# Performance work log

Hardware: AMD Instinct MI355X
Metric: run time of the kernel (lower is better)

## Reference

```python
import jax, jax.numpy as jnp
import numpy as np

B, T, DKQ, DV, EKQ, EV, H, OUT = 8, 2048, 64, 64, 128, 128, 4, 32
FF = 4 * EV
NEG = -1e30  # additive mask value (safe stand-in for -inf)


def _ln(x, g, b, eps=1e-5):
    m = x.mean(-1, keepdims=True)
    var = ((x - m) ** 2).mean(-1, keepdims=True)
    return (x - m) * jax.lax.rsqrt(var + eps) * g + b


def _attn(q, k, v, mask):
    # q,k,v: [n, T, E] -> heads [n, H, T, dh]; NOTE: no 1/sqrt(d) scaling (faithful to source)
    n, t, _ = q.shape
    q = q.reshape(n, t, H, -1).transpose(0, 2, 1, 3)
    k = k.reshape(n, t, H, -1).transpose(0, 2, 1, 3)
    v = v.reshape(n, t, H, -1).transpose(0, 2, 1, 3)
    w = jnp.einsum('bhqd,bhkd->bhqk', q, k) + mask  # [n,H,T,T]
    a = jax.nn.softmax(w, axis=-1)
    o = jnp.einsum('bhqk,bhkd->bhqd', a, v)
    return o.transpose(0, 2, 1, 3).reshape(n, t, -1)


def setup_inputs() -> dict:
    key = jax.random.key(0)
    ks = jax.random.split(key, 32)
    w = lambda k, s: jax.random.normal(k, s, jnp.float32) * 0.02
    DIN_A = DKQ + DV
    return {
        'kq': jax.random.normal(ks[0], (B, T, DKQ), jnp.float32),
        'v': jax.random.normal(ks[1], (B, T, DV), jnp.float32),
        # Layer A (input_dim = DKQ+DV, embed = EV)
        'A_Wk': w(ks[2], (DIN_A, EV)), 'A_bk': jnp.zeros((EV,), jnp.float32),
        'A_Wq': w(ks[3], (DIN_A, EV)), 'A_bq': jnp.zeros((EV,), jnp.float32),
        'A_Wv': w(ks[4], (DIN_A, EV)), 'A_bv': jnp.zeros((EV,), jnp.float32),
        'A_f1W': w(ks[5], (EV, FF)), 'A_f1b': jnp.zeros((FF,), jnp.float32),
        'A_f2W': w(ks[6], (FF, EV)), 'A_f2b': jnp.zeros((EV,), jnp.float32),
        'A_n1g': jnp.ones((EV,), jnp.float32), 'A_n1b': jnp.zeros((EV,), jnp.float32),
        'A_n2g': jnp.ones((EV,), jnp.float32), 'A_n2b': jnp.zeros((EV,), jnp.float32),
        # Layer B (kq -> EKQ, vA -> EV)
        'B_Wk': w(ks[7], (DKQ, EKQ)), 'B_bk': jnp.zeros((EKQ,), jnp.float32),
        'B_Wq': w(ks[8], (DKQ, EKQ)), 'B_bq': jnp.zeros((EKQ,), jnp.float32),
        'B_Wv': w(ks[9], (EV, EV)), 'B_bv': jnp.zeros((EV,), jnp.float32),
        'B_f1W': w(ks[10], (EV, FF)), 'B_f1b': jnp.zeros((FF,), jnp.float32),
        'B_f2W': w(ks[11], (FF, EV)), 'B_f2b': jnp.zeros((EV,), jnp.float32),
        # Output head
        'out_W': w(ks[12], (EV, OUT)), 'out_b': jnp.zeros((OUT,), jnp.float32),
    }


def reference(kq, v, A_Wk, A_bk, A_Wq, A_bq, A_Wv, A_bv, A_f1W, A_f1b, A_f2W, A_f2b,
              A_n1g, A_n1b, A_n2g, A_n2b, B_Wk, B_bk, B_Wq, B_bq, B_Wv, B_bv,
              B_f1W, B_f1b, B_f2W, B_f2b, out_W, out_b):
    n, t, _ = kq.shape
    i = jnp.arange(t)[:, None]
    j = jnp.arange(t)[None, :]
    mask_a = jnp.where(j <= i, 0.0, NEG).astype(jnp.float32)               # causal (diag=1)
    mask_b = jnp.where((j < i) | ((i == 0) & (j == 0)), 0.0, NEG).astype(jnp.float32)  # strict causal + (0,0) exception

    # ---- Layer A ----
    X = jnp.concatenate([kq, v], axis=-1)
    K = X @ A_Wk + A_bk
    Q = X @ A_Wq + A_bq
    V = X @ A_Wv + A_bv
    attn_out = _attn(Q, K, V, mask_a)
    h1 = _ln(V + attn_out, A_n1g, A_n1b)
    ff = jax.nn.gelu(h1 @ A_f1W + A_f1b, approximate=False) @ A_f2W + A_f2b
    vA = _ln(h1 + ff, A_n2g, A_n2b)

    # ---- Layer B (no residuals / norms: values is overwritten in source) ----
    K2 = kq @ B_Wk + B_bk
    Q2 = kq @ B_Wq + B_bq
    V2 = vA @ B_Wv + B_bv
    attn_out2 = _attn(Q2, K2, V2, mask_b)
    ff2 = jax.nn.gelu(attn_out2 @ B_f1W + B_f1b, approximate=False) @ B_f2W + B_f2b

    return ff2 @ out_W + out_b
```

## Files before the change

kernel.cpp:

```cpp
#include <hip/hip_runtime.h>
#include <hip/hip_bf16.h>

#define TSEQ 2048
#define NBATCH 8
#define NROWS (NBATCH*TSEQ)
#define EMB 128
#define NH 4
#define DH 32
#define OUTD 32
#define APLANE (NROWS*EMB)
#define LOG2E 1.4426950408889634f

typedef short s8v __attribute__((ext_vector_type(8)));
typedef short s4v __attribute__((ext_vector_type(4)));
typedef float f4v __attribute__((ext_vector_type(4)));

__device__ __forceinline__ unsigned short f2bf(float f){
  unsigned int u = __float_as_uint(f);
  unsigned int r = u + 0x7fffu + ((u >> 16) & 1u);
  return (unsigned short)(r >> 16);
}
__device__ __forceinline__ float bf2f(unsigned short u){
  return __uint_as_float(((unsigned int)u) << 16);
}

struct WPack {
  const float* src[10];
  int off[10];
  int ntk[10];
  int rowoff[10];
  int nsh[10];
  int kn[10];
};
__global__ __launch_bounds__(256) void prep_w(WPack p, short* __restrict__ warena){
  int blk = blockIdx.x, m = 0;
  #pragma unroll
  for (int i=0;i<10;i++){
    int nb = p.kn[i] >> 8;
    if (blk < nb){ m = i; break; }
    blk -= nb;
  }
  int idx = blk*256 + threadIdx.x;
  float x = p.src[m][idx];
  int nsh = p.nsh[m];
  int n = idx & ((1<<nsh)-1);
  int k = idx >> nsh;
  int K = p.kn[m] >> nsh;
  unsigned short hi = f2bf(x);
  unsigned short lo = f2bf(x - bf2f(hi));
  short* dh = warena + p.off[m] + (size_t)(p.rowoff[m] + n)*K + k;
  dh[0]        = (short)hi;
  dh[p.ntk[m]] = (short)lo;
}

__global__ __launch_bounds__(256) void prep_wc(const float* __restrict__ f2W, const float* __restrict__ f2b,
                                               const float* __restrict__ oW, const float* __restrict__ ob,
                                               float* __restrict__ Wc, float* __restrict__ bc){
  int idx = blockIdx.x*256 + threadIdx.x;
  if (idx < 512*32){
    int k = idx >> 5, n = idx & 31;
    float s = 0.f;
    #pragma unroll 4
    for (int j=0;j<128;j++) s = fmaf(f2W[k*128+j], oW[j*32+n], s);
    Wc[idx] = s;
  } else if (idx < 512*32 + 32){
    int n = idx - 512*32;
    float s = ob[n];
    for (int j=0;j<128;j++) s = fmaf(f2b[j], oW[j*32+n], s);
    bc[n] = s;
  }
}

__global__ __launch_bounds__(256) void xsplit(const float* __restrict__ kq, const float* __restrict__ v,
                                              unsigned short* __restrict__ X){
  int idx = blockIdx.x*256 + threadIdx.x;
  int row = idx >> 7, c = idx & 127;
  float val = (c < 64) ? kq[row*64 + c] : v[row*64 + (c-64)];
  unsigned short hi = f2bf(val);
  X[idx]          = hi;
  X[idx + APLANE] = f2bf(val - bf2f(hi));
}

struct GOuts {
  const float* bias[3];
  float* of[3];
  unsigned short* ob[3];
  unsigned short* vt[3];
  float scale[3];
};
__global__ __launch_bounds__(256) void gemm2(
    const unsigned short* __restrict__ A, int aplane, int lda, int K, int niter,
    const short* __restrict__ wt, int NTK,
    GOuts og, int NT, int nseg, int act){
  __shared__ short As[2][2][64*40];
  const int tid  = threadIdx.x;
  const int w    = tid >> 6;
  const int lane = tid & 63;
  const int col  = lane & 15;
  const int quad = lane >> 4;
  const int row0 = blockIdx.x * 64;
  const int colg = blockIdx.y*64 + w*16 + col;
  const bool two = (aplane != 0);

  f4v acc[4];
  #pragma unroll
  for (int i=0;i<4;i++) acc[i] = (f4v){0.f,0.f,0.f,0.f};

  const int ar = tid >> 2, ac = (tid & 3)*8;
  const unsigned short* abase = A + (size_t)(row0 + ar)*lda;
  const short* wbase = wt + (size_t)colg*K + quad*8;

  s8v pah, pal, pbh, pbl;
  pah = *(const s8v*)(abase + ac);
  if (two) pal = *(const s8v*)(abase + aplane + ac);
  pbh = *(const s8v*)(wbase);
  pbl = *(const s8v*)(wbase + NTK);

  for (int i=0;i<niter;i++){
    const int buf = i & 1;
    *(s8v*)&As[buf][0][ar*40 + ac] = pah;
    if (two) *(s8v*)&As[buf][1][ar*40 + ac] = pal;
    __syncthreads();
    s8v bh = pbh, bl = pbl;
    if (i+1 < niter){
      const int kcol = (i+1)*32;
      pah = *(const s8v*)(abase + kcol + ac);
      if (two) pal = *(const s8v*)(abase + aplane + kcol + ac);
      pbh = *(const s8v*)(wbase + kcol);
      pbl = *(const s8v*)(wbase + NTK + kcol);
    }
    #pragma unroll
    for (int rt=0;rt<4;rt++){
      s8v ah = *(const s8v*)&As[buf][0][(rt*16 + col)*40 + quad*8];
      acc[rt] = __builtin_amdgcn_mfma_f32_16x16x32_bf16(ah, bh, acc[rt], 0, 0, 0);
      if (two){
        s8v al = *(const s8v*)&As[buf][1][(rt*16 + col)*40 + quad*8];
        acc[rt] = __builtin_amdgcn_mfma_f32_16x16x32_bf16(al, bh, acc[rt], 0, 0, 0);
      }
      acc[rt] = __builtin_amdgcn_mfma_f32_16x16x32_bf16(ah, bl, acc[rt], 0, 0, 0);
    }
  }

  int seg, lcol, ldc;
  if (nseg > 1){ seg = colg >> 7; lcol = colg & 127; ldc = 128; }
  else         { seg = 0; lcol = colg; ldc = NT; }
  const float bv = og.bias[seg][lcol];
  const float sc = og.scale[seg];
  float* of = og.of[seg];
  unsigned short* ob = og.ob[seg];
  unsigned short* vtp = og.vt[seg];
  float vals[4][4];
  #pragma unroll
  for (int rt=0;rt<4;rt++){
    #pragma unroll
    for (int r=0;r<4;r++){
      float val = acc[rt][r] + bv;
      if (act == 1) val = 0.5f*val*(1.f + erff(val*0.70710678118654752440f));
      vals[rt][r] = val * sc;
    }
  }
  #pragma unroll
  for (int rt=0;rt<4;rt++){
    const int row = row0 + rt*16 + quad*4;
    #pragma unroll
    for (int r=0;r<4;r++){
      if (ob)      ob[(size_t)(row+r)*ldc + lcol] = f2bf(vals[rt][r]);
      else if (of) of[(size_t)(row+r)*ldc + lcol] = vals[rt][r];
    }
  }
  if (vtp){
    const int hh = lcol >> 5, dd = lcol & 31;
    const int bb = row0 >> 11;
    unsigned short* vbase = vtp + ((size_t)(bb*NH + hh)*32 + dd)*TSEQ + (row0 & (TSEQ-1)) + quad*4;
    #pragma unroll
    for (int rt=0;rt<4;rt++){
      s4v pk;
      #pragma unroll
      for (int r=0;r<4;r++) pk[r] = (short)f2bf(vals[rt][r]);
      *(s4v*)(vbase + rt*16) = pk;
    }
  }
}

#define KT_STRIDE 40
#define VT_STRIDE 72
#define PW_STRIDE 72
__global__ __launch_bounds__(128) void flash3(const unsigned short* __restrict__ Qb,
                                              const unsigned short* __restrict__ Kb,
                                              const unsigned short* __restrict__ Vtb,
                                              float* __restrict__ O0, float* __restrict__ O1,
                                              float* __restrict__ L0, float* __restrict__ L1,
                                              int mode){
  __shared__ short Kt[64*KT_STRIDE];
  __shared__ short Vt[32*VT_STRIDE];
  __shared__ short Pw[2][16*PW_STRIDE];
  const int tid  = threadIdx.x;
  const int w    = tid >> 6;
  const int lane = tid & 63;
  const int col  = lane & 15;
  const int quad = lane >> 4;
  const int bh = blockIdx.y;
  const int b = bh >> 2, h = bh & 3;
  const int par = blockIdx.z;
  float* Op = par ? O1 : O0;
  float* Lp = par ? L1 : L0;
  const int kr = tid >> 1, kc16 = (tid & 1)*16;
  const int vd = tid >> 2, vk16 = (tid & 3)*16;

  for (int pass = 0; pass < 2; pass++){
    const int t = pass ? blockIdx.x : (63 - blockIdx.x);
    const int qbase = t*32 + w*16;
    const int jtmax = t >> 1;
    const int qg = qbase + col;

    s8v qf = *(const s8v*)(Qb + (size_t)(b*TSEQ + qg)*EMB + h*DH + quad*8);
    f4v o0 = {0.f,0.f,0.f,0.f}, o1 = {0.f,0.f,0.f,0.f};
    float lsum = 0.f;

    if (par <= jtmax){
      s8v ka, kb2, va, vb;
      {
        const unsigned short* kp = Kb + (size_t)(b*TSEQ + par*64 + kr)*EMB + h*DH + kc16;
        ka = *(const s8v*)kp; kb2 = *(const s8v*)(kp + 8);
        const unsigned short* vp = Vtb + ((size_t)bh*32 + vd)*TSEQ + par*64 + vk16;
        va = *(const s8v*)vp; vb = *(const s8v*)(vp + 8);
      }
      for (int jt = par; jt <= jtmax; jt += 2){
        __syncthreads();
        *(s8v*)&Kt[kr*KT_STRIDE + kc16]     = ka;
        *(s8v*)&Kt[kr*KT_STRIDE + kc16 + 8] = kb2;
        *(s8v*)&Vt[vd*VT_STRIDE + vk16]     = va;
        *(s8v*)&Vt[vd*VT_STRIDE + vk16 + 8] = vb;
        __syncthreads();
        if (jt + 2 <= jtmax){
          const unsigned short* kp = Kb + (size_t)(b*TSEQ + (jt+2)*64 + kr)*EMB + h*DH + kc16;
          ka = *(const s8v*)kp; kb2 = *(const s8v*)(kp + 8);
          const unsigned short* vp = Vtb + ((size_t)bh*32 + vd)*TSEQ + (jt+2)*64 + vk16;
          va = *(const s8v*)vp; vb = *(const s8v*)(vp + 8);
        }
        f4v s[4];
        #pragma unroll
        for (int t4=0;t4<4;t4++){
          s8v kf = *(const s8v*)&Kt[(t4*16 + col)*KT_STRIDE + quad*8];
          f4v z = {0.f,0.f,0.f,0.f};
          s[t4] = __builtin_amdgcn_mfma_f32_16x16x32_bf16(kf, qf, z, 0, 0, 0);
        }
        if (jt == jtmax){
          const int j0 = jt*64;
          #pragma unroll
          for (int t4=0;t4<4;t4++){
            #pragma unroll
            for (int r=0;r<4;r++){
              const int jg = j0 + t4*16 + quad*4 + r;
              const bool ok = (mode==0) ? (jg <= qg) : ((jg < qg) || (qg==0 && jg==0));
              s[t4][r] = ok ? s[t4][r] : -1e30f;
            }
          }
        }
        #pragma unroll
        for (int t4=0;t4<4;t4++){
          s4v pk;
          #pragma unroll
          for (int r=0;r<4;r++){
            float pv = exp2f(s[t4][r]);
            lsum += pv;
            pk[r] = (short)f2bf(pv);
          }
          *(s4v*)&Pw[w][col*PW_STRIDE + t4*16 + quad*4] = pk;
        }
        #pragma unroll
        for (int kk=0;kk<2;kk++){
          s8v pf  = *(const s8v*)&Pw[w][col*PW_STRIDE + kk*32 + quad*8];
          s8v vf0 = *(const s8v*)&Vt[(col)*VT_STRIDE    + kk*32 + quad*8];
          s8v vf1 = *(const s8v*)&Vt[(16+col)*VT_STRIDE + kk*32 + quad*8];
          o0 = __builtin_amdgcn_mfma_f32_16x16x32_bf16(vf0, pf, o0, 0, 0, 0);
          o1 = __builtin_amdgcn_mfma_f32_16x16x32_bf16(vf1, pf, o1, 0, 0, 0);
        }
      }
    }
    lsum += __shfl_xor(lsum, 16);
    lsum += __shfl_xor(lsum, 32);
    float* obase = Op + (size_t)(b*TSEQ + qg)*EMB + h*DH + quad*4;
    *(float4*)(obase)      = make_float4(o0[0],o0[1],o0[2],o0[3]);
    *(float4*)(obase + 16) = make_float4(o1[0],o1[1],o1[2],o1[3]);
    if (quad == 0) Lp[(size_t)(b*TSEQ + qg)*NH + h] = lsum;
  }
}

__global__ __launch_bounds__(64) void combine_ln(const float* __restrict__ O0, const float* __restrict__ O1,
                                                 const float* __restrict__ L0, const float* __restrict__ L1,
                                                 const float* __restrict__ Vf,
                                                 const float* __restrict__ g, const float* __restrict__ bt,
                                                 unsigned short* __restrict__ outp){
  const int row = blockIdx.x;
  const int tid = threadIdx.x;
  const size_t base = (size_t)row*EMB;
  const int h0 = tid >> 5, h1i = 2 + (tid >> 5);
  const float la = L0[(size_t)row*NH + h0] + L1[(size_t)row*NH + h0];
  const float lb = L0[(size_t)row*NH + h1i] + L1[(size_t)row*NH + h1i];
  float x0 = Vf[base+tid]    + (O0[base+tid]    + O1[base+tid])    / la;
  float x1 = Vf[base+tid+64] + (O0[base+tid+64] + O1[base+tid+64]) / lb;
  float s  = x0 + x1;
  float s2 = x0*x0 + x1*x1;
  #pragma unroll
  for (int off=1; off<64; off<<=1){
    s  += __shfl_xor(s,  off);
    s2 += __shfl_xor(s2, off);
  }
  float mean = s * (1.f/128.f);
  float var  = s2 * (1.f/128.f) - mean*mean;
  float rstd = rsqrtf(var + 1e-5f);
  float y0 = (x0-mean)*rstd*g[tid]    + bt[tid];
  float y1 = (x1-mean)*rstd*g[tid+64] + bt[tid+64];
  unsigned short h0b = f2bf(y0), h1b = f2bf(y1);
  outp[base+tid]             = h0b;
  outp[base+tid+64]          = h1b;
  outp[base+tid+APLANE]      = f2bf(y0 - bf2f(h0b));
  outp[base+tid+64+APLANE]   = f2bf(y1 - bf2f(h1b));
}

__global__ __launch_bounds__(64) void ln2(const unsigned short* __restrict__ Xp, const float* __restrict__ R,
                                          const float* __restrict__ g, const float* __restrict__ bt,
                                          unsigned short* __restrict__ outp){
  const int row = blockIdx.x;
  const int tid = threadIdx.x;
  const size_t base = (size_t)row*EMB;
  float x0 = bf2f(Xp[base+tid])    + bf2f(Xp[base+tid+APLANE])    + R[base+tid];
  float x1 = bf2f(Xp[base+tid+64]) + bf2f(Xp[base+tid+64+APLANE]) + R[base+tid+64];
  float s  = x0 + x1;
  float s2 = x0*x0 + x1*x1;
  #pragma unroll
  for (int off=1; off<64; off<<=1){
    s  += __shfl_xor(s,  off);
    s2 += __shfl_xor(s2, off);
  }
  float mean = s * (1.f/128.f);
  float var  = s2 * (1.f/128.f) - mean*mean;
  float rstd = rsqrtf(var + 1e-5f);
  float y0 = (x0-mean)*rstd*g[tid]    + bt[tid];
  float y1 = (x1-mean)*rstd*g[tid+64] + bt[tid+64];
  unsigned short h0b = f2bf(y0), h1b = f2bf(y1);
  outp[base+tid]             = h0b;
  outp[base+tid+64]          = h1b;
  outp[base+tid+APLANE]      = f2bf(y0 - bf2f(h0b));
  outp[base+tid+64+APLANE]   = f2bf(y1 - bf2f(h1b));
}

__global__ __launch_bounds__(256) void combine_b(const float* __restrict__ O0, const float* __restrict__ O1,
                                                 const float* __restrict__ L0, const float* __restrict__ L1,
                                                 unsigned short* __restrict__ outp){
  const int idx = blockIdx.x*256 + threadIdx.x;
  const int row = idx >> 7, c = idx & 127, h = c >> 5;
  const float l = L0[(size_t)row*NH + h] + L1[(size_t)row*NH + h];
  const float v = (O0[idx] + O1[idx]) / l;
  unsigned short hb = f2bf(v);
  outp[idx]          = hb;
  outp[idx + APLANE] = f2bf(v - bf2f(hb));
}

__global__ __launch_bounds__(256) void out2(const unsigned short* __restrict__ mid,
                                            const float* __restrict__ Wc, const float* __restrict__ bc,
                                            float* __restrict__ out){
  __shared__ float As[8*512];
  const int tid = threadIdx.x;
  const int row0 = blockIdx.x*8;
  for (int idx = tid; idx < 8*512; idx += 256)
    As[idx] = bf2f(mid[(size_t)row0*512 + idx]);
  __syncthreads();
  const int r = tid >> 5, c = tid & 31;
  float acc = bc[c];
  const float* as = &As[r*512];
  #pragma unroll 8
  for (int k=0;k<512;k++) acc = fmaf(as[k], Wc[k*32+c], acc);
  out[(size_t)(row0+r)*OUTD + c] = acc;
}

extern "C" void kernel_launch(void* const* d_in, const int* in_sizes, int n_in,
                              void* d_out, int out_size, void* d_ws, size_t ws_size,
                              hipStream_t stream) {
  const float* kq    = (const float*)d_in[0];
  const float* v     = (const float*)d_in[1];
  const float* A_Wk  = (const float*)d_in[2];  const float* A_bk  = (const float*)d_in[3];
  const float* A_Wq  = (const float*)d_in[4];  const float* A_bq  = (const float*)d_in[5];
  const float* A_Wv  = (const float*)d_in[6];  const float* A_bv  = (const float*)d_in[7];
  const float* A_f1W = (const float*)d_in[8];  const float* A_f1b = (const float*)d_in[9];
  const float* A_f2W = (const float*)d_in[10]; const float* A_f2b = (const float*)d_in[11];
  const float* A_n1g = (const float*)d_in[12]; const float* A_n1b = (const float*)d_in[13];
  const float* A_n2g = (const float*)d_in[14]; const float* A_n2b = (const float*)d_in[15];
  const float* B_Wk  = (const float*)d_in[16]; const float* B_bk  = (const float*)d_in[17];
  const float* B_Wq  = (const float*)d_in[18]; const float* B_bq  = (const float*)d_in[19];
  const float* B_Wv  = (const float*)d_in[20]; const float* B_bv  = (const float*)d_in[21];
  const float* B_f1W = (const float*)d_in[22]; const float* B_f1b = (const float*)d_in[23];
  const float* B_f2W = (const float*)d_in[24]; const float* B_f2b = (const float*)d_in[25];
  const float* out_W = (const float*)d_in[26]; const float* out_b = (const float*)d_in[27];
  float* out = (float*)d_out;
  (void)in_sizes; (void)n_in; (void)out_size; (void)ws_size;

  char* ws = (char*)d_ws;
  const size_t MB = 1024*1024;
  short* warena = (short*)ws;
  float* Wc  = (float*)(ws + 1536*1024);
  float* bc  = (float*)(ws + 1536*1024 + 65536);
  unsigned short* Xs  = (unsigned short*)(ws + 2*MB);
  unsigned short* Qbf = (unsigned short*)(ws + 10*MB);
  unsigned short* Kbf = (unsigned short*)(ws + 14*MB);
  unsigned short* Vtb = (unsigned short*)(ws + 18*MB);
  float* Vf  = (float*)(ws + 22*MB);
  float* O0  = (float*)(ws + 30*MB);
  float* O1  = (float*)(ws + 38*MB);
  float* L0  = (float*)(ws + 46*MB);
  float* L1  = (float*)(ws + 47*MB);
  unsigned short* h1p = (unsigned short*)(ws + 48*MB);
  unsigned short* mid = (unsigned short*)(ws + 56*MB);
  float* ffo = (float*)(ws + 72*MB);
  unsigned short* vAp = (unsigned short*)(ws + 80*MB);

  WPack p;
  const float* srcs[10] = {A_Wq,A_Wk,A_Wv,A_f1W,A_f2W,B_Wq,B_Wk,B_Wv,B_f1W,B_f2W};
  int kn[10]     = {16384,16384,16384,65536,65536,8192,8192,16384,65536,65536};
  int nsh[10]    = {7,7,7,9,7,7,7,7,9,7};
  int off[10]    = {0,0,0,98304,229376,360448,360448,393216,425984,557056};
  int ntk[10]    = {49152,49152,49152,65536,65536,16384,16384,16384,65536,65536};
  int rowoff[10] = {0,128,256,0,0,0,128,0,0,0};
  int nblk = 0;
  for (int i=0;i<10;i++){
    p.src[i]=srcs[i]; p.kn[i]=kn[i]; p.nsh[i]=nsh[i];
    p.off[i]=off[i]; p.ntk[i]=ntk[i]; p.rowoff[i]=rowoff[i];
    nblk += kn[i] >> 8;
  }
  prep_w<<<nblk, 256, 0, stream>>>(p, warena);
  prep_wc<<<65, 256, 0, stream>>>(B_f2W, B_f2b, out_W, out_b, Wc, bc);
  xsplit<<<NROWS*128/256, 256, 0, stream>>>(kq, v, Xs);

  GOuts oQKVA = {{A_bq,A_bk,A_bv},{nullptr,nullptr,Vf},{Qbf,Kbf,nullptr},{nullptr,nullptr,Vtb},{LOG2E,1.f,1.f}};
  GOuts oF1A  = {{A_f1b,nullptr,nullptr},{nullptr,nullptr,nullptr},{mid,nullptr,nullptr},{nullptr,nullptr,nullptr},{1.f,1.f,1.f}};
  GOuts oF2A  = {{A_f2b,nullptr,nullptr},{ffo,nullptr,nullptr},{nullptr,nullptr,nullptr},{nullptr,nullptr,nullptr},{1.f,1.f,1.f}};
  GOuts oQKB  = {{B_bq,B_bk,nullptr},{nullptr,nullptr,nullptr},{Qbf,Kbf,nullptr},{nullptr,nullptr,nullptr},{LOG2E,1.f,1.f}};
  GOuts oVB   = {{B_bv,nullptr,nullptr},{nullptr,nullptr,nullptr},{nullptr,nullptr,nullptr},{Vtb,nullptr,nullptr},{1.f,1.f,1.f}};
  GOuts oF1B  = {{B_f1b,nullptr,nullptr},{nullptr,nullptr,nullptr},{mid,nullptr,nullptr},{nullptr,nullptr,nullptr},{1.f,1.f,1.f}};

  gemm2<<<dim3(256,6), 256, 0, stream>>>(Xs, APLANE, 128, 128, 4, warena + 0,      49152, oQKVA, 384, 3, 0);
  flash3<<<dim3(32,32,2), 128, 0, stream>>>(Qbf, Kbf, Vtb, O0, O1, L0, L1, 0);
  combine_ln<<<NROWS, 64, 0, stream>>>(O0, O1, L0, L1, Vf, A_n1g, A_n1b, h1p);
  gemm2<<<dim3(256,8), 256, 0, stream>>>(h1p, APLANE, 128, 128, 4, warena + 98304, 65536, oF1A, 512, 1, 1);
  gemm2<<<dim3(256,2), 256, 0, stream>>>(mid, 0,      512, 512, 16, warena + 229376, 65536, oF2A, 128, 1, 0);
  ln2<<<NROWS, 64, 0, stream>>>(h1p, ffo, A_n2g, A_n2b, vAp);

  gemm2<<<dim3(256,4), 256, 0, stream>>>(Xs, APLANE, 128, 64, 2,  warena + 360448, 16384, oQKB, 256, 2, 0);
  gemm2<<<dim3(256,2), 256, 0, stream>>>(vAp, APLANE, 128, 128, 4, warena + 393216, 16384, oVB, 128, 1, 0);
  flash3<<<dim3(32,32,2), 128, 0, stream>>>(Qbf, Kbf, Vtb, O0, O1, L0, L1, 1);
  combine_b<<<NROWS*128/256, 256, 0, stream>>>(O0, O1, L0, L1, h1p);
  gemm2<<<dim3(256,8), 256, 0, stream>>>(h1p, APLANE, 128, 128, 4, warena + 425984, 65536, oF1B, 512, 1, 1);
  out2<<<NROWS/8, 256, 0, stream>>>(mid, Wc, bc, out);
}
```

Measured before the change: 333.1 us.

## Merge prep kernels, move V transpose to separate kernel, compute row sums via MFMA

The three setup kernels (weight split, combined output weights, input split) are merged into one launch to cut launch overhead. The GEMM epilogue no longer writes the transposed V with scattered stores; it writes row-major bf16 V, and a new LDS-based transpose kernel produces the transposed layout. In the flash kernel the softmax row sums are computed with an extra MFMA against a ones vector instead of scalar adds and shuffles, and packing uses paired bf16 conversion. Workspace buffers are also remapped to reuse regions. This adds two small kernel launches and one extra MFMA per tile.

```diff
diff --git a/kernel.cpp b/kernel.cpp
--- a/kernel.cpp
+++ b/kernel.cpp
@@ -12,7 +12,6 @@
 #define LOG2E 1.4426950408889634f
 
 typedef short s8v __attribute__((ext_vector_type(8)));
-typedef short s4v __attribute__((ext_vector_type(4)));
 typedef float f4v __attribute__((ext_vector_type(4)));
 
 __device__ __forceinline__ unsigned short f2bf(float f){
@@ -32,60 +31,62 @@
   int nsh[10];
   int kn[10];
 };
-__global__ __launch_bounds__(256) void prep_w(WPack p, short* __restrict__ warena){
-  int blk = blockIdx.x, m = 0;
-  #pragma unroll
-  for (int i=0;i<10;i++){
-    int nb = p.kn[i] >> 8;
-    if (blk < nb){ m = i; break; }
-    blk -= nb;
-  }
-  int idx = blk*256 + threadIdx.x;
-  float x = p.src[m][idx];
-  int nsh = p.nsh[m];
-  int n = idx & ((1<<nsh)-1);
-  int k = idx >> nsh;
-  int K = p.kn[m] >> nsh;
-  unsigned short hi = f2bf(x);
-  unsigned short lo = f2bf(x - bf2f(hi));
-  short* dh = warena + p.off[m] + (size_t)(p.rowoff[m] + n)*K + k;
-  dh[0]        = (short)hi;
-  dh[p.ntk[m]] = (short)lo;
-}
-
-__global__ __launch_bounds__(256) void prep_wc(const float* __restrict__ f2W, const float* __restrict__ f2b,
-                                               const float* __restrict__ oW, const float* __restrict__ ob,
-                                               float* __restrict__ Wc, float* __restrict__ bc){
-  int idx = blockIdx.x*256 + threadIdx.x;
-  if (idx < 512*32){
-    int k = idx >> 5, n = idx & 31;
-    float s = 0.f;
-    #pragma unroll 4
-    for (int j=0;j<128;j++) s = fmaf(f2W[k*128+j], oW[j*32+n], s);
-    Wc[idx] = s;
-  } else if (idx < 512*32 + 32){
-    int n = idx - 512*32;
-    float s = ob[n];
-    for (int j=0;j<128;j++) s = fmaf(f2b[j], oW[j*32+n], s);
-    bc[n] = s;
-  }
-}
-
-__global__ __launch_bounds__(256) void xsplit(const float* __restrict__ kq, const float* __restrict__ v,
-                                              unsigned short* __restrict__ X){
-  int idx = blockIdx.x*256 + threadIdx.x;
-  int row = idx >> 7, c = idx & 127;
-  float val = (c < 64) ? kq[row*64 + c] : v[row*64 + (c-64)];
-  unsigned short hi = f2bf(val);
-  X[idx]          = hi;
-  X[idx + APLANE] = f2bf(val - bf2f(hi));
+struct PrepArgs {
+  const float* f2W; const float* f2b; const float* oW; const float* ob;
+  float* Wc; float* bc;
+  const float* kq; const float* v;
+  unsigned short* X;
+  int nblk_w;
+};
+__global__ __launch_bounds__(256) void prep_all(WPack p, PrepArgs a, short* __restrict__ warena){
+  int bid = blockIdx.x;
+  if (bid < a.nblk_w){
+    int blk = bid, m = 0;
+    #pragma unroll
+    for (int i=0;i<10;i++){
+      int nb = p.kn[i] >> 8;
+      if (blk < nb){ m = i; break; }
+      blk -= nb;
+    }
+    int idx = blk*256 + threadIdx.x;
+    float x = p.src[m][idx];
+    int nsh = p.nsh[m];
+    int n = idx & ((1<<nsh)-1);
+    int k = idx >> nsh;
+    int K = p.kn[m] >> nsh;
+    unsigned short hi = f2bf(x);
+    unsigned short lo = f2bf(x - bf2f(hi));
+    short* dh = warena + p.off[m] + (size_t)(p.rowoff[m] + n)*K + k;
+    dh[0]        = (short)hi;
+    dh[p.ntk[m]] = (short)lo;
+  } else if (bid < a.nblk_w + 65){
+    int idx = (bid - a.nblk_w)*256 + threadIdx.x;
+    if (idx < 512*32){
+      int k = idx >> 5, n = idx & 31;
+      float s = 0.f;
+      #pragma unroll 4
+      for (int j=0;j<128;j++) s = fmaf(a.f2W[k*128+j], a.oW[j*32+n], s);
+      a.Wc[idx] = s;
+    } else if (idx < 512*32 + 32){
+      int n = idx - 512*32;
+      float s = a.ob[n];
+      for (int j=0;j<128;j++) s = fmaf(a.f2b[j], a.oW[j*32+n], s);
+      a.bc[n] = s;
+    }
+  } else {
+    int idx = (bid - a.nblk_w - 65)*256 + threadIdx.x;
+    int row = idx >> 7, c = idx & 127;
+    float val = (c < 64) ? a.kq[row*64 + c] : a.v[row*64 + (c-64)];
+    unsigned short hi = f2bf(val);
+    a.X[idx]          = hi;
+    a.X[idx + APLANE] = f2bf(val - bf2f(hi));
+  }
 }
 
 struct GOuts {
   const float* bias[3];
   float* of[3];
   unsigned short* ob[3];
-  unsigned short* vt[3];
   float scale[3];
 };
 __global__ __launch_bounds__(256) void gemm2(
@@ -148,44 +149,43 @@
   const float sc = og.scale[seg];
   float* of = og.of[seg];
   unsigned short* ob = og.ob[seg];
-  unsigned short* vtp = og.vt[seg];
-  float vals[4][4];
   #pragma unroll
   for (int rt=0;rt<4;rt++){
     #pragma unroll
     for (int r=0;r<4;r++){
+      const int row = row0 + rt*16 + quad*4 + r;
       float val = acc[rt][r] + bv;
       if (act == 1) val = 0.5f*val*(1.f + erff(val*0.70710678118654752440f));
-      vals[rt][r] = val * sc;
-    }
-  }
-  #pragma unroll
-  for (int rt=0;rt<4;rt++){
-    const int row = row0 + rt*16 + quad*4;
-    #pragma unroll
-    for (int r=0;r<4;r++){
-      if (ob)      ob[(size_t)(row+r)*ldc + lcol] = f2bf(vals[rt][r]);
-      else if (of) of[(size_t)(row+r)*ldc + lcol] = vals[rt][r];
-    }
-  }
-  if (vtp){
-    const int hh = lcol >> 5, dd = lcol & 31;
-    const int bb = row0 >> 11;
-    unsigned short* vbase = vtp + ((size_t)(bb*NH + hh)*32 + dd)*TSEQ + (row0 & (TSEQ-1)) + quad*4;
-    #pragma unroll
-    for (int rt=0;rt<4;rt++){
-      s4v pk;
-      #pragma unroll
-      for (int r=0;r<4;r++) pk[r] = (short)f2bf(vals[rt][r]);
-      *(s4v*)(vbase + rt*16) = pk;
-    }
-  }
+      val *= sc;
+      if (ob) ob[(size_t)row*ldc + lcol] = f2bf(val);
+      if (of) of[(size_t)row*ldc + lcol] = val;
+    }
+  }
+}
+
+__global__ __launch_bounds__(256) void vtrans2(const unsigned short* __restrict__ Vbf,
+                                               unsigned short* __restrict__ Vtb){
+  __shared__ short Lt[64*40];
+  const int tid = threadIdx.x;
+  const int t0 = blockIdx.x * 64;
+  const int bh = blockIdx.y;
+  const int b = bh >> 2, h = bh & 3;
+  {
+    const int r = tid >> 2, c = (tid & 3)*8;
+    *(s8v*)&Lt[r*40 + c] = *(const s8v*)(Vbf + (size_t)(b*TSEQ + t0 + r)*EMB + h*DH + c);
+  }
+  __syncthreads();
+  const int d = tid >> 3, kc = (tid & 7)*8;
+  s8v o;
+  #pragma unroll
+  for (int j=0;j<8;j++) o[j] = Lt[(kc + j)*40 + d];
+  *(s8v*)(Vtb + ((size_t)bh*32 + d)*TSEQ + t0 + kc) = o;
 }
 
 #define KT_STRIDE 40
 #define VT_STRIDE 72
 #define PW_STRIDE 72
-__global__ __launch_bounds__(128) void flash3(const unsigned short* __restrict__ Qb,
+__global__ __launch_bounds__(128) void flash5(const unsigned short* __restrict__ Qb,
                                               const unsigned short* __restrict__ Kb,
                                               const unsigned short* __restrict__ Vtb,
                                               float* __restrict__ O0, float* __restrict__ O1,
@@ -206,6 +206,9 @@
   float* Lp = par ? L1 : L0;
   const int kr = tid >> 1, kc16 = (tid & 1)*16;
   const int vd = tid >> 2, vk16 = (tid & 3)*16;
+  s8v ones;
+  #pragma unroll
+  for (int j=0;j<8;j++) ones[j] = (short)0x3F80;
 
   for (int pass = 0; pass < 2; pass++){
     const int t = pass ? blockIdx.x : (63 - blockIdx.x);
@@ -214,8 +217,7 @@
     const int qg = qbase + col;
 
     s8v qf = *(const s8v*)(Qb + (size_t)(b*TSEQ + qg)*EMB + h*DH + quad*8);
-    f4v o0 = {0.f,0.f,0.f,0.f}, o1 = {0.f,0.f,0.f,0.f};
-    float lsum = 0.f;
+    f4v o0 = {0,0,0,0}, o1 = {0,0,0,0}, lacc = {0,0,0,0};
 
     if (par <= jtmax){
       s8v ka, kb2, va, vb;
@@ -239,10 +241,10 @@
           va = *(const s8v*)vp; vb = *(const s8v*)(vp + 8);
         }
         f4v s[4];
+        f4v z = {0,0,0,0};
         #pragma unroll
         for (int t4=0;t4<4;t4++){
           s8v kf = *(const s8v*)&Kt[(t4*16 + col)*KT_STRIDE + quad*8];
-          f4v z = {0.f,0.f,0.f,0.f};
           s[t4] = __builtin_amdgcn_mfma_f32_16x16x32_bf16(kf, qf, z, 0, 0, 0);
         }
         if (jt == jtmax){
@@ -259,31 +261,32 @@
         }
         #pragma unroll
         for (int t4=0;t4<4;t4++){
-          s4v pk;
-          #pragma unroll
-          for (int r=0;r<4;r++){
-            float pv = exp2f(s[t4][r]);
-            lsum += pv;
-            pk[r] = (short)f2bf(pv);
-          }
-          *(s4v*)&Pw[w][col*PW_STRIDE + t4*16 + quad*4] = pk;
+          float p0 = exp2f(s[t4][0]);
+          float p1 = exp2f(s[t4][1]);
+          float p2 = exp2f(s[t4][2]);
+          float p3 = exp2f(s[t4][3]);
+          __hip_bfloat162 c01 = __float22bfloat162_rn(make_float2(p0, p1));
+          __hip_bfloat162 c23 = __float22bfloat162_rn(make_float2(p2, p3));
+          int2 pk;
+          pk.x = *reinterpret_cast<int*>(&c01);
+          pk.y = *reinterpret_cast<int*>(&c23);
+          *(int2*)&Pw[w][col*PW_STRIDE + t4*16 + quad*4] = pk;
         }
         #pragma unroll
         for (int kk=0;kk<2;kk++){
           s8v pf  = *(const s8v*)&Pw[w][col*PW_STRIDE + kk*32 + quad*8];
           s8v vf0 = *(const s8v*)&Vt[(col)*VT_STRIDE    + kk*32 + quad*8];
           s8v vf1 = *(const s8v*)&Vt[(16+col)*VT_STRIDE + kk*32 + quad*8];
-          o0 = __builtin_amdgcn_mfma_f32_16x16x32_bf16(vf0, pf, o0, 0, 0, 0);
-          o1 = __builtin_amdgcn_mfma_f32_16x16x32_bf16(vf1, pf, o1, 0, 0, 0);
+          o0   = __builtin_amdgcn_mfma_f32_16x16x32_bf16(vf0, pf, o0, 0, 0, 0);
+          o1   = __builtin_amdgcn_mfma_f32_16x16x32_bf16(vf1, pf, o1, 0, 0, 0);
+          lacc = __builtin_amdgcn_mfma_f32_16x16x32_bf16(ones, pf, lacc, 0, 0, 0);
         }
       }
     }
-    lsum += __shfl_xor(lsum, 16);
-    lsum += __shfl_xor(lsum, 32);
-    float* obase = Op + (size_t)(b*TSEQ + qg)*EMB + h*DH + quad*4;
-    *(float4*)(obase)      = make_float4(o0[0],o0[1],o0[2],o0[3]);
-    *(float4*)(obase + 16) = make_float4(o1[0],o1[1],o1[2],o1[3]);
-    if (quad == 0) Lp[(size_t)(b*TSEQ + qg)*NH + h] = lsum;
+    float* ob = Op + (size_t)(b*TSEQ + qg)*EMB + h*DH + quad*4;
+    *(float4*)(ob)      = make_float4(o0[0],o0[1],o0[2],o0[3]);
+    *(float4*)(ob + 16) = make_float4(o1[0],o1[1],o1[2],o1[3]);
+    if (quad == 0) Lp[(size_t)(b*TSEQ + qg)*NH + h] = lacc[0];
   }
 }
 
@@ -296,8 +299,9 @@
   const int tid = threadIdx.x;
   const size_t base = (size_t)row*EMB;
   const int h0 = tid >> 5, h1i = 2 + (tid >> 5);
-  const float la = L0[(size_t)row*NH + h0] + L1[(size_t)row*NH + h0];
-  const float lb = L0[(size_t)row*NH + h1i] + L1[(size_t)row*NH + h1i];
+  const size_t lb0 = (size_t)row*NH;
+  const float la = L0[lb0+h0] + L1[lb0+h0];
+  const float lb = L0[lb0+h1i] + L1[lb0+h1i];
   float x0 = Vf[base+tid]    + (O0[base+tid]    + O1[base+tid])    / la;
   float x1 = Vf[base+tid+64] + (O0[base+tid+64] + O1[base+tid+64]) / lb;
   float s  = x0 + x1;
@@ -351,7 +355,8 @@
                                                  unsigned short* __restrict__ outp){
   const int idx = blockIdx.x*256 + threadIdx.x;
   const int row = idx >> 7, c = idx & 127, h = c >> 5;
-  const float l = L0[(size_t)row*NH + h] + L1[(size_t)row*NH + h];
+  const size_t lb = (size_t)row*NH + h;
+  const float l = L0[lb] + L1[lb];
   const float v = (O0[idx] + O1[idx]) / l;
   unsigned short hb = f2bf(v);
   outp[idx]          = hb;
@@ -405,15 +410,16 @@
   unsigned short* Qbf = (unsigned short*)(ws + 10*MB);
   unsigned short* Kbf = (unsigned short*)(ws + 14*MB);
   unsigned short* Vtb = (unsigned short*)(ws + 18*MB);
-  float* Vf  = (float*)(ws + 22*MB);
-  float* O0  = (float*)(ws + 30*MB);
-  float* O1  = (float*)(ws + 38*MB);
-  float* L0  = (float*)(ws + 46*MB);
-  float* L1  = (float*)(ws + 47*MB);
-  unsigned short* h1p = (unsigned short*)(ws + 48*MB);
-  unsigned short* mid = (unsigned short*)(ws + 56*MB);
-  float* ffo = (float*)(ws + 72*MB);
-  unsigned short* vAp = (unsigned short*)(ws + 80*MB);
+  unsigned short* Vbf = (unsigned short*)(ws + 22*MB);
+  float* Vf  = (float*)(ws + 26*MB);
+  float* O0  = (float*)(ws + 34*MB);
+  float* O1  = (float*)(ws + 42*MB);
+  float* L0  = (float*)(ws + 50*MB);
+  float* L1  = (float*)(ws + 50*MB + 262144);
+  unsigned short* h1p = (unsigned short*)(ws + 51*MB);
+  unsigned short* mid = (unsigned short*)(ws + 59*MB);
+  float* ffo = (float*)(ws + 34*MB);
+  unsigned short* vAp = (unsigned short*)(ws + 42*MB);
 
   WPack p;
   const float* srcs[10] = {A_Wq,A_Wk,A_Wv,A_f1W,A_f2W,B_Wq,B_Wk,B_Wv,B_f1W,B_f2W};
@@ -422,34 +428,37 @@
   int off[10]    = {0,0,0,98304,229376,360448,360448,393216,425984,557056};
   int ntk[10]    = {49152,49152,49152,65536,65536,16384,16384,16384,65536,65536};
   int rowoff[10] = {0,128,256,0,0,0,128,0,0,0};
-  int nblk = 0;
+  int nblk_w = 0;
   for (int i=0;i<10;i++){
     p.src[i]=srcs[i]; p.kn[i]=kn[i]; p.nsh[i]=nsh[i];
     p.off[i]=off[i]; p.ntk[i]=ntk[i]; p.rowoff[i]=rowoff[i];
-    nblk += kn[i] >> 8;
-  }
-  prep_w<<<nblk, 256, 0, stream>>>(p, warena);
-  prep_wc<<<65, 256, 0, stream>>>(B_f2W, B_f2b, out_W, out_b, Wc, bc);
-  xsplit<<<NROWS*128/256, 256, 0, stream>>>(kq, v, Xs);
-
-  GOuts oQKVA = {{A_bq,A_bk,A_bv},{nullptr,nullptr,Vf},{Qbf,Kbf,nullptr},{nullptr,nullptr,Vtb},{LOG2E,1.f,1.f}};
-  GOuts oF1A  = {{A_f1b,nullptr,nullptr},{nullptr,nullptr,nullptr},{mid,nullptr,nullptr},{nullptr,nullptr,nullptr},{1.f,1.f,1.f}};
-  GOuts oF2A  = {{A_f2b,nullptr,nullptr},{ffo,nullptr,nullptr},{nullptr,nullptr,nullptr},{nullptr,nullptr,nullptr},{1.f,1.f,1.f}};
-  GOuts oQKB  = {{B_bq,B_bk,nullptr},{nullptr,nullptr,nullptr},{Qbf,Kbf,nullptr},{nullptr,nullptr,nullptr},{LOG2E,1.f,1.f}};
-  GOuts oVB   = {{B_bv,nullptr,nullptr},{nullptr,nullptr,nullptr},{nullptr,nullptr,nullptr},{Vtb,nullptr,nullptr},{1.f,1.f,1.f}};
-  GOuts oF1B  = {{B_f1b,nullptr,nullptr},{nullptr,nullptr,nullptr},{mid,nullptr,nullptr},{nullptr,nullptr,nullptr},{1.f,1.f,1.f}};
+    nblk_w += kn[i] >> 8;
+  }
+  PrepArgs pa;
+  pa.f2W = B_f2W; pa.f2b = B_f2b; pa.oW = out_W; pa.ob = out_b;
+  pa.Wc = Wc; pa.bc = bc; pa.kq = kq; pa.v = v; pa.X = Xs; pa.nblk_w = nblk_w;
+  prep_all<<<nblk_w + 65 + NROWS*128/256, 256, 0, stream>>>(p, pa, warena);
+
+  GOuts oQKVA = {{A_bq,A_bk,A_bv},{nullptr,nullptr,Vf},{Qbf,Kbf,Vbf},{LOG2E,1.f,1.f}};
+  GOuts oF1A  = {{A_f1b,nullptr,nullptr},{nullptr,nullptr,nullptr},{mid,nullptr,nullptr},{1.f,1.f,1.f}};
+  GOuts oF2A  = {{A_f2b,nullptr,nullptr},{ffo,nullptr,nullptr},{nullptr,nullptr,nullptr},{1.f,1.f,1.f}};
+  GOuts oQKB  = {{B_bq,B_bk,nullptr},{nullptr,nullptr,nullptr},{Qbf,Kbf,nullptr},{LOG2E,1.f,1.f}};
+  GOuts oVB   = {{B_bv,nullptr,nullptr},{nullptr,nullptr,nullptr},{Vbf,nullptr,nullptr},{1.f,1.f,1.f}};
+  GOuts oF1B  = {{B_f1b,nullptr,nullptr},{nullptr,nullptr,nullptr},{mid,nullptr,nullptr},{1.f,1.f,1.f}};
 
   gemm2<<<dim3(256,6), 256, 0, stream>>>(Xs, APLANE, 128, 128, 4, warena + 0,      49152, oQKVA, 384, 3, 0);
-  flash3<<<dim3(32,32,2), 128, 0, stream>>>(Qbf, Kbf, Vtb, O0, O1, L0, L1, 0);
-  combine_ln<<<NROWS, 64, 0, stream>>>(O0, O1, L0, L1, Vf, A_n1g, A_n1b, h1p);
+  vtrans2<<<dim3(32,32), 256, 0, stream>>>(Vbf, Vtb);
+  flash5<<<dim3(32,32,2), 128, 0, stream>>>(Qbf, Kbf, Vtb, O0,O1, L0,L1, 0);
+  combine_ln<<<NROWS, 64, 0, stream>>>(O0,O1, L0,L1, Vf, A_n1g, A_n1b, h1p);
   gemm2<<<dim3(256,8), 256, 0, stream>>>(h1p, APLANE, 128, 128, 4, warena + 98304, 65536, oF1A, 512, 1, 1);
   gemm2<<<dim3(256,2), 256, 0, stream>>>(mid, 0,      512, 512, 16, warena + 229376, 65536, oF2A, 128, 1, 0);
   ln2<<<NROWS, 64, 0, stream>>>(h1p, ffo, A_n2g, A_n2b, vAp);
 
   gemm2<<<dim3(256,4), 256, 0, stream>>>(Xs, APLANE, 128, 64, 2,  warena + 360448, 16384, oQKB, 256, 2, 0);
   gemm2<<<dim3(256,2), 256, 0, stream>>>(vAp, APLANE, 128, 128, 4, warena + 393216, 16384, oVB, 128, 1, 0);
-  flash3<<<dim3(32,32,2), 128, 0, stream>>>(Qbf, Kbf, Vtb, O0, O1, L0, L1, 1);
-  combine_b<<<NROWS*128/256, 256, 0, stream>>>(O0, O1, L0, L1, h1p);
+  vtrans2<<<dim3(32,32), 256, 0, stream>>>(Vbf, Vtb);
+  flash5<<<dim3(32,32,2), 128, 0, stream>>>(Qbf, Kbf, Vtb, O0,O1, L0,L1, 1);
+  combine_b<<<NROWS*128/256, 256, 0, stream>>>(O0,O1, L0,L1, h1p);
   gemm2<<<dim3(256,8), 256, 0, stream>>>(h1p, APLANE, 128, 128, 4, warena + 425984, 65536, oF1B, 512, 1, 1);
   out2<<<NROWS/8, 256, 0, stream>>>(mid, Wc, bc, out);
 }
```

Result: faster. 326.0 us (-2.1%).
